# Performance work log

Hardware: AMD Instinct MI355X
Metric: run time of the kernel (lower is better)

## Reference

```python
import jax, jax.numpy as jnp
import numpy as np

USER_NUM, ITEM_NUM = 50000, 25000
N_U, N_I = 4096, 4096
N_E, N_PRED = 262144, 65536
D, K, N_LAYERS = 64, 1000, 3
SSL_TEMP, SSL_REG, ALPHA, PROTO_REG = 0.1, 1e-6, 1.0, 8e-8


def setup_inputs() -> dict:
    key = jax.random.key(0)
    ks = jax.random.split(key, 16)
    return {
        "emb_user": jax.random.normal(ks[0], (USER_NUM, D), jnp.float32),
        "emb_item": jax.random.normal(ks[1], (ITEM_NUM, D), jnp.float32),
        "user_centroids": jax.random.normal(ks[2], (K, D), jnp.float32),
        "item_centroids": jax.random.normal(ks[3], (K, D), jnp.float32),
        "edge_u": jax.random.randint(ks[4], (N_E,), 0, N_U, jnp.int32),
        "edge_v": jax.random.randint(ks[5], (N_E,), 0, N_I, jnp.int32),
        "pos_u": jax.random.randint(ks[6], (N_PRED,), 0, N_U, jnp.int32),
        "pos_v": jax.random.randint(ks[7], (N_PRED,), 0, N_I, jnp.int32),
        "neg_u": jax.random.randint(ks[8], (N_PRED,), 0, N_U, jnp.int32),
        "neg_v": jax.random.randint(ks[9], (N_PRED,), 0, N_I, jnp.int32),
        "idx_user": jax.random.randint(ks[10], (N_U,), 0, USER_NUM, jnp.int32),
        "idx_item": jax.random.randint(ks[11], (N_I,), 0, ITEM_NUM, jnp.int32),
        "user2cluster": jax.random.randint(ks[12], (USER_NUM,), 0, K, jnp.int32),
        "item2cluster": jax.random.randint(ks[13], (ITEM_NUM,), 0, K, jnp.int32),
    }


def _l2norm(x, eps=1e-12):  # F.normalize(p=2, dim=1)
    return x / jnp.maximum(jnp.linalg.norm(x, axis=1, keepdims=True), eps)


def _ssl_loss(cur, prev, prev_total):
    nc, npv, nt = _l2norm(cur), _l2norm(prev), _l2norm(prev_total)
    pos = jnp.exp(jnp.sum(nc * npv, axis=1) / SSL_TEMP)            # [B]
    tot = jnp.exp(nc @ nt.T / SSL_TEMP).sum(axis=1)                 # [B]
    return -jnp.log(pos / tot).sum()


def _proto_loss(emb, idx, node2cluster, centroids):
    ne = _l2norm(emb)
    cents = _l2norm(centroids)                                      # run_kmeans normalizes centroids
    my_cent = cents[node2cluster[idx]]                              # [B, D]
    pos = jnp.exp(jnp.sum(ne * my_cent, axis=1) / SSL_TEMP)
    tot = jnp.exp(ne @ cents.T / SSL_TEMP).sum(axis=1)
    return -jnp.log(pos / tot).sum()


def reference(emb_user, emb_item, user_centroids, item_centroids,
              edge_u, edge_v, pos_u, pos_v, neg_u, neg_v,
              idx_user, idx_item, user2cluster, item2cluster):
    # --- symmetric-normalized bipartite GraphConv (norm='both', no weight/bias) ---
    ones_e = jnp.ones((N_E,), jnp.float32)
    deg_u = jax.ops.segment_sum(ones_e, edge_u, num_segments=N_U)
    deg_i = jax.ops.segment_sum(ones_e, edge_v, num_segments=N_I)
    inv_u = (1.0 / jnp.sqrt(jnp.maximum(deg_u, 1.0)))[:, None]      # [N_U,1]
    inv_i = (1.0 / jnp.sqrt(jnp.maximum(deg_i, 1.0)))[:, None]      # [N_I,1]

    e_u = emb_user[idx_user]                                        # initial subgraph embeddings
    e_i = emb_item[idx_item]
    res_u, res_i = e_u, e_i
    h_u, h_i = e_u, e_i
    for _ in range(N_LAYERS):
        m_u = (h_u * inv_u)[edge_u]                                 # messages along rate edges
        m_i = (h_i * inv_i)[edge_v]                                 # messages along rated-by edges
        new_i = jax.ops.segment_sum(m_u, edge_v, num_segments=N_I) * inv_i
        new_u = jax.ops.segment_sum(m_i, edge_u, num_segments=N_U) * inv_u
        h_u, h_i = new_u, new_i
        res_u = res_u + h_u
        res_i = res_i + h_i

    # --- structural-neighbour SSL loss (last layer output vs layer-0 embeddings) ---
    ssl_u = _ssl_loss(h_u, e_u, emb_user)
    ssl_i = _ssl_loss(h_i, e_i, emb_item)
    ssl_loss = SSL_REG * (ssl_u + ALPHA * ssl_i)

    # --- protoNCE loss (raw embedding-table rows vs kmeans centroids) ---
    proto_loss = PROTO_REG * (
        _proto_loss(emb_user[idx_user], idx_user, user2cluster, user_centroids)
        + _proto_loss(emb_item[idx_item], idx_item, item2cluster, item_centroids)
    )

    res_u = res_u / (N_LAYERS + 1)
    res_i = res_i / (N_LAYERS + 1)

    # --- HeteroDotProductPredictor: u_dot_v on 'rate' edges -> [E,1] ---
    pos_score = jnp.sum(res_u[pos_u] * res_i[pos_v], axis=1, keepdims=True)
    neg_score = jnp.sum(res_u[neg_u] * res_i[neg_v], axis=1, keepdims=True)
    return pos_score, neg_score, ssl_loss, proto_loss
```

## Files before the change

### kernel.cpp

```cpp
#include <hip/hip_runtime.h>
#include <hip/hip_bf16.h>

#define NU 4096
#define NI 4096
#define NE 262144
#define NPRED 65536
#define DD 64
#define KCL 1000
#define UNUM 50000
#define INUM 25000
#define INUM_PAD 25008
#define KCL_PAD 1008

typedef short sh8 __attribute__((ext_vector_type(8)));
typedef float f4 __attribute__((ext_vector_type(4)));

__device__ __forceinline__ float wred64(float x){
#pragma unroll
  for(int m=1;m<64;m<<=1) x += __shfl_xor(x,m);
  return x;
}

__device__ __forceinline__ float fast_exp2(float x){
  return __builtin_amdgcn_exp2f(x);
}

__global__ void k_hist(const int* __restrict__ eu, const int* __restrict__ ev,
                       int* cu, int* ci){
  int t = blockIdx.x*256 + threadIdx.x;
  if(t < NE){ atomicAdd(&cu[eu[t]],1); atomicAdd(&ci[ev[t]],1); }
}

__global__ void k_scan(const int* cnt_u, int* rp_u, int* cur_u, float* inv_u,
                       const int* cnt_i, int* rp_i, int* cur_i, float* inv_i){
  const int* cnt = blockIdx.x ? cnt_i : cnt_u;
  int* rp  = blockIdx.x ? rp_i  : rp_u;
  int* cur = blockIdx.x ? cur_i : cur_u;
  float* inv = blockIdx.x ? inv_i : inv_u;
  __shared__ int sdata[1024];
  int tid = threadIdx.x;
  int v[4]; int s = 0;
#pragma unroll
  for(int k=0;k<4;k++){ v[k]=cnt[tid*4+k]; s+=v[k]; }
  sdata[tid]=s; __syncthreads();
  for(int off=1; off<1024; off<<=1){
    int add = (tid>=off)? sdata[tid-off] : 0;
    __syncthreads();
    if(tid>=off) sdata[tid] += add;
    __syncthreads();
  }
  int run = sdata[tid]-s;
#pragma unroll
  for(int k=0;k<4;k++){
    int idx = tid*4+k;
    rp[idx]=run; cur[idx]=run;
    inv[idx] = 1.0f/sqrtf(fmaxf((float)v[k],1.0f));
    run += v[k];
  }
  if(tid==1023) rp[4096]=run;
}

__global__ void k_fill(const int* __restrict__ eu, const int* __restrict__ ev,
                       int* cur_u, int* cur_i, int* adj_u, int* adj_i){
  int t = blockIdx.x*256 + threadIdx.x;
  if(t < NE){
    int u=eu[t], v=ev[t];
    adj_u[atomicAdd(&cur_u[u],1)] = v;
    adj_i[atomicAdd(&cur_i[v],1)] = u;
  }
}

__global__ void k_gather(const float* __restrict__ emb_u, const float* __restrict__ emb_i,
                         const int* __restrict__ idx_u, const int* __restrict__ idx_i,
                         const float* __restrict__ inv_u, const float* __restrict__ inv_i,
                         float* e_u, float* e_i, float* res_u, float* res_i,
                         float* hs_u, float* hs_i){
  int t = blockIdx.x*256 + threadIdx.x;
  const int half = NU*DD;
  if(t < half){
    int r=t>>6;
    float v = emb_u[idx_u[r]*DD + (t&63)];
    e_u[t]=v; res_u[t]=v; hs_u[t]=v*inv_u[r];
  } else {
    int s=t-half; int r=s>>6;
    float v = emb_i[idx_i[r]*DD + (s&63)];
    e_i[s]=v; res_i[s]=v; hs_i[s]=v*inv_i[r];
  }
}

__global__ void k_conv(const int* __restrict__ rp_i, const int* __restrict__ adj_i,
                       const float* __restrict__ hsu_in, const float* __restrict__ inv_i,
                       float* h_i, float* res_i, float* hsi_out,
                       const int* __restrict__ rp_u, const int* __restrict__ adj_u,
                       const float* __restrict__ hsi_in, const float* __restrict__ inv_u,
                       float* h_u, float* res_u, float* hsu_out){
  int b = blockIdx.x*4 + (threadIdx.x>>6);
  int lane = threadIdx.x & 63;
  const int* rp; const int* adj; const float* srcv; const float* inv;
  float *h, *res, *hso; int node;
  if(b < NI){ rp=rp_i; adj=adj_i; srcv=hsu_in; inv=inv_i; h=h_i; res=res_i; hso=hsi_out; node=b; }
  else      { node=b-NI; rp=rp_u; adj=adj_u; srcv=hsi_in; inv=inv_u; h=h_u; res=res_u; hso=hsu_out; }
  int s=rp[node], e=rp[node+1];
  float acc=0.f;
  for(int base=s; base<e; base+=64){
    int m = e-base;
    int myidx = adj[base + min(lane, m-1)];
    int kk = min(64, m);
    int k=0;
    for(; k+8<=kk; k+=8){
      int i0=__shfl(myidx,k  ), i1=__shfl(myidx,k+1),
          i2=__shfl(myidx,k+2), i3=__shfl(myidx,k+3),
          i4=__shfl(myidx,k+4), i5=__shfl(myidx,k+5),
          i6=__shfl(myidx,k+6), i7=__shfl(myidx,k+7);
      float v0=srcv[i0*DD+lane], v1=srcv[i1*DD+lane],
            v2=srcv[i2*DD+lane], v3=srcv[i3*DD+lane],
            v4=srcv[i4*DD+lane], v5=srcv[i5*DD+lane],
            v6=srcv[i6*DD+lane], v7=srcv[i7*DD+lane];
      acc += ((v0+v1)+(v2+v3)) + ((v4+v5)+(v6+v7));
    }
    for(; k<kk; k++) acc += srcv[__shfl(myidx,k)*DD+lane];
  }
  float iv = inv[node];
  float outv = acc*iv;
  h[node*DD+lane] = outv;
  res[node*DD+lane] += outv;
  hso[node*DD+lane] = outv*iv;
}

#define SB0 12500
#define SB1 (SB0+6252)
#define SB2 (SB1+252)
#define SB3 (SB2+252)
#define SB4 (SB3+1024)
#define SB5 (SB4+1024)
#define SB6 (SB5+1024)
#define SB7 (SB6+1024)

__global__ void k_normall(const float* __restrict__ emb_u, const float* __restrict__ emb_i,
                          const float* __restrict__ ucent, const float* __restrict__ icent,
                          const float* __restrict__ h_u, const float* __restrict__ h_i,
                          const float* __restrict__ e_u, const float* __restrict__ e_i,
                          __hip_bfloat16* ntb_u, __hip_bfloat16* ntb_i,
                          __hip_bfloat16* ncb_u, __hip_bfloat16* ncb_i,
                          __hip_bfloat16* nc_u, __hip_bfloat16* nc_i,
                          __hip_bfloat16* npv_u, __hip_bfloat16* npv_i){
  const float SC = 14.426950408889634f;
  int b = blockIdx.x;
  const float* in; __hip_bfloat16* outp; int rows; float scale; int base;
  if(b < SB0)      { in=emb_u; outp=ntb_u; rows=UNUM; scale=1.f;  base=0; }
  else if(b < SB1) { in=emb_i; outp=ntb_i; rows=INUM; scale=1.f;  base=SB0; }
  else if(b < SB2) { in=ucent; outp=ncb_u; rows=KCL;  scale=1.f;  base=SB1; }
  else if(b < SB3) { in=icent; outp=ncb_i; rows=KCL;  scale=1.f;  base=SB2; }
  else if(b < SB4) { in=h_u;   outp=nc_u;  rows=NU;   scale=SC;   base=SB3; }
  else if(b < SB5) { in=h_i;   outp=nc_i;  rows=NI;   scale=SC;   base=SB4; }
  else if(b < SB6) { in=e_u;   outp=npv_u; rows=NU;   scale=SC;   base=SB5; }
  else             { in=e_i;   outp=npv_i; rows=NI;   scale=SC;   base=SB6; }
  int row = (b-base)*4 + (threadIdx.x>>6);
  int lane = threadIdx.x & 63;
  if(row >= rows){
    outp[row*DD + lane] = __float2bfloat16(0.f);
    return;
  }
  float v = in[row*DD + lane];
  float s = wred64(v*v);
  float sc = scale / fmaxf(sqrtf(s), 1e-12f);
  outp[row*DD + lane] = __float2bfloat16(v*sc);
}

__global__ void k_pos(const float* __restrict__ h_u, const float* __restrict__ h_i,
                      const float* __restrict__ e_u, const float* __restrict__ e_i,
                      const float* __restrict__ cent_u, const float* __restrict__ cent_i,
                      const int* __restrict__ idx_u, const int* __restrict__ idx_i,
                      const int* __restrict__ u2c, const int* __restrict__ i2c,
                      float* pos4){
  int w = blockIdx.x*4 + (threadIdx.x>>6);
  int lane = threadIdx.x & 63;
  if(w >= NU) return;
  float hu=h_u[w*DD+lane], eu=e_u[w*DD+lane];
  float hi=h_i[w*DD+lane], ei=e_i[w*DD+lane];
  int cu = u2c[idx_u[w]], ci = i2c[idx_i[w]];
  float cuv = cent_u[cu*DD+lane], civ = cent_i[ci*DD+lane];
  float hh = wred64(hu*hu), ee = wred64(eu*eu), he = wred64(hu*eu);
  float h2 = wred64(hi*hi), e2 = wred64(ei*ei), hei= wred64(hi*ei);
  float ccu= wred64(cuv*cuv), ecu = wred64(eu*cuv);
  float cci= wred64(civ*civ), eci = wred64(ei*civ);
  if(lane==0){
    const float eps=1e-12f;
    pos4[0*NU+w] = he  / (fmaxf(sqrtf(hh),eps)*fmaxf(sqrtf(ee),eps));
    pos4[1*NU+w] = hei / (fmaxf(sqrtf(h2),eps)*fmaxf(sqrtf(e2),eps));
    pos4[2*NU+w] = ecu / (fmaxf(sqrtf(ee),eps)*fmaxf(sqrtf(ccu),eps));
    pos4[3*NU+w] = eci / (fmaxf(sqrtf(e2),eps)*fmaxf(sqrtf(cci),eps));
  }
}

#define ECH 256
#define EU0 1568
#define EU1 (EU0+784)
#define EU2 (EU1+32)
#define EU3 (EU2+32)

struct ESeg { const __hip_bfloat16* A; const __hip_bfloat16* B; float* tot; int nB; };

__global__ __launch_bounds__(256,4)
void k_expsum(ESeg s0, ESeg s1, ESeg s2, ESeg s3){
  int wave = threadIdx.x >> 6;
  int lane = threadIdx.x & 63;
  int r = lane & 15, kq = (lane>>4)*8;

  for(int u = blockIdx.x; u < EU3; u += 1024){
    ESeg s; int rem;
    if(u < EU0)      { s = s0; rem = u; }
    else if(u < EU1) { s = s1; rem = u-EU0; }
    else if(u < EU2) { s = s2; rem = u-EU1; }
    else             { s = s3; rem = u-EU2; }
    int yc = rem >> 3, x = rem & 7;
    int row0 = (x*4 + wave)*128;
    int j_begin = yc*ECH;
    int j_end = min(j_begin + ECH, s.nB);

    sh8 a0[8], a1[8];
#pragma unroll
    for(int t=0;t<8;t++){
      const short* ap = (const short*)(s.A + (row0 + t*16 + r)*DD);
      a0[t] = *(const sh8*)(ap + kq);
      a1[t] = *(const sh8*)(ap + kq + 32);
    }
    float acc[8][4];
#pragma unroll
    for(int t=0;t<8;t++)
#pragma unroll
      for(int q=0;q<4;q++) acc[t][q]=0.f;

    const short* bbase = (const short*)s.B;
    const short* bp0 = bbase + (j_begin + r)*DD + kq;
    sh8 b0 = *(const sh8*)(bp0);
    sh8 b1 = *(const sh8*)(bp0 + 32);

#pragma unroll 2
    for(int j0=j_begin; j0<j_end; j0+=16){
      const short* np = bbase + (j0 + 16 + r)*DD + kq;
      sh8 n0 = *(const sh8*)(np);
      sh8 n1 = *(const sh8*)(np + 32);
#pragma unroll
      for(int t=0;t<8;t++){
        f4 c = {0.f,0.f,0.f,0.f};
        c = __builtin_amdgcn_mfma_f32_16x16x32_bf16(a0[t], b0, c, 0,0,0);
        c = __builtin_amdgcn_mfma_f32_16x16x32_bf16(a1[t], b1, c, 0,0,0);
#pragma unroll
        for(int q=0;q<4;q++) acc[t][q] += fast_exp2(c[q]);
      }
      b0 = n0; b1 = n1;
    }
#pragma unroll
    for(int t=0;t<8;t++){
#pragma unroll
      for(int q=0;q<4;q++){
        float v = acc[t][q];
        v += __shfl_xor(v,1); v += __shfl_xor(v,2);
        v += __shfl_xor(v,4); v += __shfl_xor(v,8);
        if(r==0) atomicAdd(&s.tot[row0 + t*16 + (lane>>4)*4 + q], v);
      }
    }
  }
}

__global__ void k_score(const float* __restrict__ res_u, const float* __restrict__ res_i,
                        const int* __restrict__ pu, const int* __restrict__ pv,
                        const int* __restrict__ nu, const int* __restrict__ nv,
                        float* out){
  int t = blockIdx.x*256 + threadIdx.x;
  int pair = t >> 4;
  int sl = t & 15;
  if(pair >= 2*NPRED) return;
  int a,b;
  if(pair < NPRED){ a=pu[pair]; b=pv[pair]; }
  else { a=nu[pair-NPRED]; b=nv[pair-NPRED]; }
  f4 xu = *(const f4*)(res_u + a*DD + sl*4);
  f4 xv = *(const f4*)(res_i + b*DD + sl*4);
  float x = xu[0]*xv[0] + xu[1]*xv[1] + xu[2]*xv[2] + xu[3]*xv[3];
  x += __shfl_xor(x,1); x += __shfl_xor(x,2);
  x += __shfl_xor(x,4); x += __shfl_xor(x,8);
  if(sl==0) out[pair] = x*(1.0f/16.0f);
}

__global__ void k_loss(const float* __restrict__ tot4, const float* __restrict__ pos4,
                       float* out){
  const float PI_ = (float)(INUM_PAD-INUM), PK_ = (float)(KCL_PAD-KCL);
  float s0=0,s1=0,s2=0,s3=0;
  for(int b=threadIdx.x; b<NU; b+=256){
    s0 += logf(tot4[0*NU+b])       - 10.f*pos4[0*NU+b];
    s1 += logf(tot4[1*NU+b] - PI_) - 10.f*pos4[1*NU+b];
    s2 += logf(tot4[2*NU+b] - PK_) - 10.f*pos4[2*NU+b];
    s3 += logf(tot4[3*NU+b] - PK_) - 10.f*pos4[3*NU+b];
  }
  s0=wred64(s0); s1=wred64(s1); s2=wred64(s2); s3=wred64(s3);
  __shared__ float ls[4][4];
  int lane=threadIdx.x&63, w=threadIdx.x>>6;
  if(lane==0){ ls[w][0]=s0; ls[w][1]=s1; ls[w][2]=s2; ls[w][3]=s3; }
  __syncthreads();
  if(threadIdx.x==0){
    float a=0,b2=0,c=0,d=0;
#pragma unroll
    for(int k=0;k<4;k++){ a+=ls[k][0]; b2+=ls[k][1]; c+=ls[k][2]; d+=ls[k][3]; }
    out[2*NPRED]   = 1e-6f*(a+b2);
    out[2*NPRED+1] = 8e-8f*(c+d);
  }
}

extern "C" void kernel_launch(void* const* d_in, const int* in_sizes, int n_in,
                              void* d_out, int out_size, void* d_ws, size_t ws_size,
                              hipStream_t stream) {
  const float* emb_user = (const float*)d_in[0];
  const float* emb_item = (const float*)d_in[1];
  const float* ucent    = (const float*)d_in[2];
  const float* icent    = (const float*)d_in[3];
  const int* edge_u = (const int*)d_in[4];
  const int* edge_v = (const int*)d_in[5];
  const int* pos_u  = (const int*)d_in[6];
  const int* pos_v  = (const int*)d_in[7];
  const int* neg_u  = (const int*)d_in[8];
  const int* neg_v  = (const int*)d_in[9];
  const int* idx_u  = (const int*)d_in[10];
  const int* idx_i  = (const int*)d_in[11];
  const int* u2c    = (const int*)d_in[12];
  const int* i2c    = (const int*)d_in[13];
  float* out = (float*)d_out;

  char* w = (char*)d_ws;
  auto alloc = [&](size_t bytes)->void*{
    void* p = (void*)w;
    w += (bytes + 255) & ~(size_t)255;
    return p;
  };
  int* cnt_u = (int*)alloc(NU*4);
  int* cnt_i = (int*)alloc(NI*4);
  int* rp_u  = (int*)alloc((NU+1)*4);
  int* rp_i  = (int*)alloc((NI+1)*4);
  int* cur_u = (int*)alloc(NU*4);
  int* cur_i = (int*)alloc(NI*4);
  int* adj_u = (int*)alloc((size_t)NE*4);
  int* adj_i = (int*)alloc((size_t)NE*4);
  float* inv_u = (float*)alloc(NU*4);
  float* inv_i = (float*)alloc(NI*4);
  float* e_u  = (float*)alloc((size_t)NU*DD*4);
  float* e_i  = (float*)alloc((size_t)NI*DD*4);
  float* h_u  = (float*)alloc((size_t)NU*DD*4);
  float* h_i  = (float*)alloc((size_t)NI*DD*4);
  float* hsA_u = (float*)alloc((size_t)NU*DD*4);
  float* hsA_i = (float*)alloc((size_t)NI*DD*4);
  float* hsB_u = (float*)alloc((size_t)NU*DD*4);
  float* hsB_i = (float*)alloc((size_t)NI*DD*4);
  float* res_u= (float*)alloc((size_t)NU*DD*4);
  float* res_i= (float*)alloc((size_t)NI*DD*4);
  __hip_bfloat16* ntb_user = (__hip_bfloat16*)alloc((size_t)(UNUM+48)*DD*2);
  __hip_bfloat16* ntb_item = (__hip_bfloat16*)alloc((size_t)(INUM_PAD+48)*DD*2);
  __hip_bfloat16* ncb_u = (__hip_bfloat16*)alloc((size_t)(KCL_PAD+48)*DD*2);
  __hip_bfloat16* ncb_i = (__hip_bfloat16*)alloc((size_t)(KCL_PAD+48)*DD*2);
  __hip_bfloat16* nc_u  = (__hip_bfloat16*)alloc((size_t)NU*DD*2);
  __hip_bfloat16* nc_i  = (__hip_bfloat16*)alloc((size_t)NI*DD*2);
  __hip_bfloat16* npv_u = (__hip_bfloat16*)alloc((size_t)NU*DD*2);
  __hip_bfloat16* npv_i = (__hip_bfloat16*)alloc((size_t)NI*DD*2);
  float* tot4 = (float*)alloc(4*NU*4);
  float* pos4 = (float*)alloc(4*NU*4);

  hipMemsetAsync(cnt_u, 0, NU*4, stream);
  hipMemsetAsync(cnt_i, 0, NI*4, stream);
  hipMemsetAsync(tot4, 0, 4*NU*4, stream);

  k_hist<<<NE/256, 256, 0, stream>>>(edge_u, edge_v, cnt_u, cnt_i);
  k_scan<<<2, 1024, 0, stream>>>(cnt_u, rp_u, cur_u, inv_u, cnt_i, rp_i, cur_i, inv_i);
  k_fill<<<NE/256, 256, 0, stream>>>(edge_u, edge_v, cur_u, cur_i, adj_u, adj_i);
  k_gather<<<2*NU*DD/256, 256, 0, stream>>>(emb_user, emb_item, idx_u, idx_i,
                                            inv_u, inv_i,
                                            e_u, e_i, res_u, res_i, hsA_u, hsA_i);
  k_conv<<<(NU+NI)/4, 256, 0, stream>>>(rp_i, adj_i, hsA_u, inv_i, h_i, res_i, hsB_i,
                                        rp_u, adj_u, hsA_i, inv_u, h_u, res_u, hsB_u);
  k_conv<<<(NU+NI)/4, 256, 0, stream>>>(rp_i, adj_i, hsB_u, inv_i, h_i, res_i, hsA_i,
                                        rp_u, adj_u, hsB_i, inv_u, h_u, res_u, hsA_u);
  k_conv<<<(NU+NI)/4, 256, 0, stream>>>(rp_i, adj_i, hsA_u, inv_i, h_i, res_i, hsB_i,
                                        rp_u, adj_u, hsA_i, inv_u, h_u, res_u, hsB_u);

  k_normall<<<SB7, 256, 0, stream>>>(emb_user, emb_item, ucent, icent,
                                     h_u, h_i, e_u, e_i,
                                     ntb_user, ntb_item, ncb_u, ncb_i,
                                     nc_u, nc_i, npv_u, npv_i);

  k_pos<<<NU/4, 256, 0, stream>>>(h_u, h_i, e_u, e_i, ucent, icent,
                                  idx_u, idx_i, u2c, i2c, pos4);

  ESeg su = { nc_u,  ntb_user, tot4 + 0*NU, UNUM };
  ESeg si = { nc_i,  ntb_item, tot4 + 1*NU, INUM_PAD };
  ESeg sp0= { npv_u, ncb_u,    tot4 + 2*NU, KCL_PAD };
  ESeg sp1= { npv_i, ncb_i,    tot4 + 3*NU, KCL_PAD };
  k_expsum<<<1024, 256, 0, stream>>>(su, si, sp0, sp1);

  k_score<<<(2*NPRED*16)/256, 256, 0, stream>>>(res_u, res_i, pos_u, pos_v, neg_u, neg_v, out);
  k_loss<<<1, 256, 0, stream>>>(tot4, pos4, out);
}
```

Measured before the change: 241.2 us.

## Fuse small kernels and widen exp-sum inner loop to 32 columns

```diff
diff --git a/kernel.cpp b/kernel.cpp
--- a/kernel.cpp
+++ b/kernel.cpp
@@ -9,8 +9,9 @@
 #define KCL 1000
 #define UNUM 50000
 #define INUM 25000
-#define INUM_PAD 25008
-#define KCL_PAD 1008
+#define NUPAD 50016
+#define NIPAD 25024
+#define NKPAD 1024
 
 typedef short sh8 __attribute__((ext_vector_type(8)));
 typedef float f4 __attribute__((ext_vector_type(4)));
@@ -32,7 +33,13 @@
 }
 
 __global__ void k_scan(const int* cnt_u, int* rp_u, int* cur_u, float* inv_u,
-                       const int* cnt_i, int* rp_i, int* cur_i, float* inv_i){
+                       const int* cnt_i, int* rp_i, int* cur_i, float* inv_i,
+                       float* tot4){
+  {
+    int base = blockIdx.x*8192 + threadIdx.x*8;
+#pragma unroll
+    for(int k=0;k<8;k++) tot4[base+k] = 0.f;
+  }
   const int* cnt = blockIdx.x ? cnt_i : cnt_u;
   int* rp  = blockIdx.x ? rp_i  : rp_u;
   int* cur = blockIdx.x ? cur_i : cur_u;
@@ -60,31 +67,31 @@
   if(tid==1023) rp[4096]=run;
 }
 
-__global__ void k_fill(const int* __restrict__ eu, const int* __restrict__ ev,
-                       int* cur_u, int* cur_i, int* adj_u, int* adj_i){
-  int t = blockIdx.x*256 + threadIdx.x;
-  if(t < NE){
+__global__ void k_fillgather(const int* __restrict__ eu, const int* __restrict__ ev,
+                             int* cur_u, int* cur_i, int* adj_u, int* adj_i,
+                             const float* __restrict__ emb_u, const float* __restrict__ emb_i,
+                             const int* __restrict__ idx_u, const int* __restrict__ idx_i,
+                             const float* __restrict__ inv_u, const float* __restrict__ inv_i,
+                             float* e_u, float* e_i, float* res_u, float* res_i,
+                             float* hs_u, float* hs_i){
+  int b = blockIdx.x;
+  if(b < 1024){
+    int t = b*256 + threadIdx.x;
     int u=eu[t], v=ev[t];
     adj_u[atomicAdd(&cur_u[u],1)] = v;
     adj_i[atomicAdd(&cur_i[v],1)] = u;
-  }
-}
-
-__global__ void k_gather(const float* __restrict__ emb_u, const float* __restrict__ emb_i,
-                         const int* __restrict__ idx_u, const int* __restrict__ idx_i,
-                         const float* __restrict__ inv_u, const float* __restrict__ inv_i,
-                         float* e_u, float* e_i, float* res_u, float* res_i,
-                         float* hs_u, float* hs_i){
-  int t = blockIdx.x*256 + threadIdx.x;
-  const int half = NU*DD;
-  if(t < half){
-    int r=t>>6;
-    float v = emb_u[idx_u[r]*DD + (t&63)];
-    e_u[t]=v; res_u[t]=v; hs_u[t]=v*inv_u[r];
   } else {
-    int s=t-half; int r=s>>6;
-    float v = emb_i[idx_i[r]*DD + (s&63)];
-    e_i[s]=v; res_i[s]=v; hs_i[s]=v*inv_i[r];
+    int t = (b-1024)*256 + threadIdx.x;
+    const int half = NU*DD;
+    if(t < half){
+      int r=t>>6;
+      float v = emb_u[idx_u[r]*DD + (t&63)];
+      e_u[t]=v; res_u[t]=v; hs_u[t]=v*inv_u[r];
+    } else {
+      int s=t-half; int r=s>>6;
+      float v = emb_i[idx_i[r]*DD + (s&63)];
+      e_i[s]=v; res_i[s]=v; hs_i[s]=v*inv_i[r];
+    }
   }
 }
 
@@ -127,25 +134,48 @@
   hso[node*DD+lane] = outv*iv;
 }
 
-#define SB0 12500
-#define SB1 (SB0+6252)
-#define SB2 (SB1+252)
-#define SB3 (SB2+252)
+#define SB0 12504
+#define SB1 (SB0+6256)
+#define SB2 (SB1+256)
+#define SB3 (SB2+256)
 #define SB4 (SB3+1024)
 #define SB5 (SB4+1024)
 #define SB6 (SB5+1024)
 #define SB7 (SB6+1024)
 
-__global__ void k_normall(const float* __restrict__ emb_u, const float* __restrict__ emb_i,
+__global__ void k_normpos(const float* __restrict__ emb_u, const float* __restrict__ emb_i,
                           const float* __restrict__ ucent, const float* __restrict__ icent,
                           const float* __restrict__ h_u, const float* __restrict__ h_i,
                           const float* __restrict__ e_u, const float* __restrict__ e_i,
                           __hip_bfloat16* ntb_u, __hip_bfloat16* ntb_i,
                           __hip_bfloat16* ncb_u, __hip_bfloat16* ncb_i,
                           __hip_bfloat16* nc_u, __hip_bfloat16* nc_i,
-                          __hip_bfloat16* npv_u, __hip_bfloat16* npv_i){
+                          __hip_bfloat16* npv_u, __hip_bfloat16* npv_i,
+                          const int* __restrict__ idx_u, const int* __restrict__ idx_i,
+                          const int* __restrict__ u2c, const int* __restrict__ i2c,
+                          float* pos4){
   const float SC = 14.426950408889634f;
   int b = blockIdx.x;
+  int lane = threadIdx.x & 63;
+  if(b >= SB7){
+    int w = (b-SB7)*4 + (threadIdx.x>>6);
+    float hu=h_u[w*DD+lane], eu=e_u[w*DD+lane];
+    float hi=h_i[w*DD+lane], ei=e_i[w*DD+lane];
+    int cu = u2c[idx_u[w]], ci = i2c[idx_i[w]];
+    float cuv = ucent[cu*DD+lane], civ = icent[ci*DD+lane];
+    float hh = wred64(hu*hu), ee = wred64(eu*eu), he = wred64(hu*eu);
+    float h2 = wred64(hi*hi), e2 = wred64(ei*ei), hei= wred64(hi*ei);
+    float ccu= wred64(cuv*cuv), ecu = wred64(eu*cuv);
+    float cci= wred64(civ*civ), eci = wred64(ei*civ);
+    if(lane==0){
+      const float eps=1e-12f;
+      pos4[0*NU+w] = he  / (fmaxf(sqrtf(hh),eps)*fmaxf(sqrtf(ee),eps));
+      pos4[1*NU+w] = hei / (fmaxf(sqrtf(h2),eps)*fmaxf(sqrtf(e2),eps));
+      pos4[2*NU+w] = ecu / (fmaxf(sqrtf(ee),eps)*fmaxf(sqrtf(ccu),eps));
+      pos4[3*NU+w] = eci / (fmaxf(sqrtf(e2),eps)*fmaxf(sqrtf(cci),eps));
+    }
+    return;
+  }
   const float* in; __hip_bfloat16* outp; int rows; float scale; int base;
   if(b < SB0)      { in=emb_u; outp=ntb_u; rows=UNUM; scale=1.f;  base=0; }
   else if(b < SB1) { in=emb_i; outp=ntb_i; rows=INUM; scale=1.f;  base=SB0; }
@@ -156,7 +186,6 @@
   else if(b < SB6) { in=e_u;   outp=npv_u; rows=NU;   scale=SC;   base=SB5; }
   else             { in=e_i;   outp=npv_i; rows=NI;   scale=SC;   base=SB6; }
   int row = (b-base)*4 + (threadIdx.x>>6);
-  int lane = threadIdx.x & 63;
   if(row >= rows){
     outp[row*DD + lane] = __float2bfloat16(0.f);
     return;
@@ -167,128 +196,113 @@
   outp[row*DD + lane] = __float2bfloat16(v*sc);
 }
 
-__global__ void k_pos(const float* __restrict__ h_u, const float* __restrict__ h_i,
-                      const float* __restrict__ e_u, const float* __restrict__ e_i,
-                      const float* __restrict__ cent_u, const float* __restrict__ cent_i,
-                      const int* __restrict__ idx_u, const int* __restrict__ idx_i,
-                      const int* __restrict__ u2c, const int* __restrict__ i2c,
-                      float* pos4){
-  int w = blockIdx.x*4 + (threadIdx.x>>6);
-  int lane = threadIdx.x & 63;
-  if(w >= NU) return;
-  float hu=h_u[w*DD+lane], eu=e_u[w*DD+lane];
-  float hi=h_i[w*DD+lane], ei=e_i[w*DD+lane];
-  int cu = u2c[idx_u[w]], ci = i2c[idx_i[w]];
-  float cuv = cent_u[cu*DD+lane], civ = cent_i[ci*DD+lane];
-  float hh = wred64(hu*hu), ee = wred64(eu*eu), he = wred64(hu*eu);
-  float h2 = wred64(hi*hi), e2 = wred64(ei*ei), hei= wred64(hi*ei);
-  float ccu= wred64(cuv*cuv), ecu = wred64(eu*cuv);
-  float cci= wred64(civ*civ), eci = wred64(ei*civ);
-  if(lane==0){
-    const float eps=1e-12f;
-    pos4[0*NU+w] = he  / (fmaxf(sqrtf(hh),eps)*fmaxf(sqrtf(ee),eps));
-    pos4[1*NU+w] = hei / (fmaxf(sqrtf(h2),eps)*fmaxf(sqrtf(e2),eps));
-    pos4[2*NU+w] = ecu / (fmaxf(sqrtf(ee),eps)*fmaxf(sqrtf(ccu),eps));
-    pos4[3*NU+w] = eci / (fmaxf(sqrtf(e2),eps)*fmaxf(sqrtf(cci),eps));
-  }
-}
-
 #define ECH 256
-#define EU0 1568
-#define EU1 (EU0+784)
-#define EU2 (EU1+32)
-#define EU3 (EU2+32)
+#define EUU 1568
+#define EUI (EUU+784)
+#define EUP0 (EUI+32)
+#define EUP1 (EUP0+32)
+#define NSU 8192
+#define UTOT (EUP1+NSU)
 
 struct ESeg { const __hip_bfloat16* A; const __hip_bfloat16* B; float* tot; int nB; };
-
-__global__ __launch_bounds__(256,4)
-void k_expsum(ESeg s0, ESeg s1, ESeg s2, ESeg s3){
-  int wave = threadIdx.x >> 6;
-  int lane = threadIdx.x & 63;
+struct SArg { const float* res_u; const float* res_i;
+              const int* pu; const int* pv; const int* nu; const int* nv; float* out; };
+
+__global__ __launch_bounds__(256,3)
+void k_expscore(ESeg s0, ESeg s1, ESeg s2, ESeg s3, SArg sc){
+  int tid = threadIdx.x;
+  int wave = tid >> 6;
+  int lane = tid & 63;
   int r = lane & 15, kq = (lane>>4)*8;
 
-  for(int u = blockIdx.x; u < EU3; u += 1024){
-    ESeg s; int rem;
-    if(u < EU0)      { s = s0; rem = u; }
-    else if(u < EU1) { s = s1; rem = u-EU0; }
-    else if(u < EU2) { s = s2; rem = u-EU1; }
-    else             { s = s3; rem = u-EU2; }
-    int yc = rem >> 3, x = rem & 7;
-    int row0 = (x*4 + wave)*128;
-    int j_begin = yc*ECH;
-    int j_end = min(j_begin + ECH, s.nB);
-
-    sh8 a0[8], a1[8];
-#pragma unroll
-    for(int t=0;t<8;t++){
-      const short* ap = (const short*)(s.A + (row0 + t*16 + r)*DD);
-      a0[t] = *(const sh8*)(ap + kq);
-      a1[t] = *(const sh8*)(ap + kq + 32);
+  for(int u = blockIdx.x; u < UTOT; u += 1024){
+    if(u < EUP1){
+      ESeg s; int rem;
+      if(u < EUU)       { s = s0; rem = u; }
+      else if(u < EUI)  { s = s1; rem = u-EUU; }
+      else if(u < EUP0) { s = s2; rem = u-EUI; }
+      else              { s = s3; rem = u-EUP0; }
+      int yc = rem >> 3, x = rem & 7;
+      int row0 = (x*4 + wave)*128;
+      int j_begin = yc*ECH;
+      int j_end = min(j_begin + ECH, s.nB);
+
+      sh8 a0[8], a1[8];
+#pragma unroll
+      for(int t=0;t<8;t++){
+        const short* ap = (const short*)(s.A + (row0 + t*16 + r)*DD);
+        a0[t] = *(const sh8*)(ap + kq);
+        a1[t] = *(const sh8*)(ap + kq + 32);
+      }
+      float acc[8][4];
+#pragma unroll
+      for(int t=0;t<8;t++)
+#pragma unroll
+        for(int q=0;q<4;q++) acc[t][q]=0.f;
+
+      const short* bbase = (const short*)s.B;
+      const short* bp = bbase + (j_begin + r)*DD + kq;
+      sh8 b0 = *(const sh8*)(bp);
+      sh8 b1 = *(const sh8*)(bp + 32);
+      sh8 b2 = *(const sh8*)(bp + 16*DD);
+      sh8 b3 = *(const sh8*)(bp + 16*DD + 32);
+
+#pragma unroll 1
+      for(int j0=j_begin; j0<j_end; j0+=32){
+        const short* np = bbase + (j0 + 32 + r)*DD + kq;
+        sh8 n0 = *(const sh8*)(np);
+        sh8 n1 = *(const sh8*)(np + 32);
+        sh8 n2 = *(const sh8*)(np + 16*DD);
+        sh8 n3 = *(const sh8*)(np + 16*DD + 32);
+#pragma unroll
+        for(int t=0;t<8;t++){
+          f4 c0 = {0.f,0.f,0.f,0.f};
+          f4 c1 = {0.f,0.f,0.f,0.f};
+          c0 = __builtin_amdgcn_mfma_f32_16x16x32_bf16(a0[t], b0, c0, 0,0,0);
+          c1 = __builtin_amdgcn_mfma_f32_16x16x32_bf16(a0[t], b2, c1, 0,0,0);
+          c0 = __builtin_amdgcn_mfma_f32_16x16x32_bf16(a1[t], b1, c0, 0,0,0);
+          c1 = __builtin_amdgcn_mfma_f32_16x16x32_bf16(a1[t], b3, c1, 0,0,0);
+#pragma unroll
+          for(int q=0;q<4;q++)
+            acc[t][q] += fast_exp2(c0[q]) + fast_exp2(c1[q]);
+        }
+        b0 = n0; b1 = n1; b2 = n2; b3 = n3;
+      }
+#pragma unroll
+      for(int t=0;t<8;t++){
+#pragma unroll
+        for(int q=0;q<4;q++){
+          float v = acc[t][q];
+          v += __shfl_xor(v,1); v += __shfl_xor(v,2);
+          v += __shfl_xor(v,4); v += __shfl_xor(v,8);
+          if(r==0) atomicAdd(&s.tot[row0 + t*16 + (lane>>4)*4 + q], v);
+        }
+      }
+    } else {
+      int u2 = u - EUP1;
+      int pair = u2*16 + (tid>>4);
+      int sl = tid & 15;
+      int a,b;
+      if(pair < NPRED){ a=sc.pu[pair]; b=sc.pv[pair]; }
+      else { a=sc.nu[pair-NPRED]; b=sc.nv[pair-NPRED]; }
+      f4 xu = *(const f4*)(sc.res_u + a*DD + sl*4);
+      f4 xv = *(const f4*)(sc.res_i + b*DD + sl*4);
+      float x = xu[0]*xv[0] + xu[1]*xv[1] + xu[2]*xv[2] + xu[3]*xv[3];
+      x += __shfl_xor(x,1); x += __shfl_xor(x,2);
+      x += __shfl_xor(x,4); x += __shfl_xor(x,8);
+      if(sl==0) sc.out[pair] = x*(1.0f/16.0f);
     }
-    float acc[8][4];
-#pragma unroll
-    for(int t=0;t<8;t++)
-#pragma unroll
-      for(int q=0;q<4;q++) acc[t][q]=0.f;
-
-    const short* bbase = (const short*)s.B;
-    const short* bp0 = bbase + (j_begin + r)*DD + kq;
-    sh8 b0 = *(const sh8*)(bp0);
-    sh8 b1 = *(const sh8*)(bp0 + 32);
-
-#pragma unroll 2
-    for(int j0=j_begin; j0<j_end; j0+=16){
-      const short* np = bbase + (j0 + 16 + r)*DD + kq;
-      sh8 n0 = *(const sh8*)(np);
-      sh8 n1 = *(const sh8*)(np + 32);
-#pragma unroll
-      for(int t=0;t<8;t++){
-        f4 c = {0.f,0.f,0.f,0.f};
-        c = __builtin_amdgcn_mfma_f32_16x16x32_bf16(a0[t], b0, c, 0,0,0);
-        c = __builtin_amdgcn_mfma_f32_16x16x32_bf16(a1[t], b1, c, 0,0,0);
-#pragma unroll
-        for(int q=0;q<4;q++) acc[t][q] += fast_exp2(c[q]);
-      }
-      b0 = n0; b1 = n1;
-    }
-#pragma unroll
-    for(int t=0;t<8;t++){
-#pragma unroll
-      for(int q=0;q<4;q++){
-        float v = acc[t][q];
-        v += __shfl_xor(v,1); v += __shfl_xor(v,2);
-        v += __shfl_xor(v,4); v += __shfl_xor(v,8);
-        if(r==0) atomicAdd(&s.tot[row0 + t*16 + (lane>>4)*4 + q], v);
-      }
-    }
-  }
-}
-
-__global__ void k_score(const float* __restrict__ res_u, const float* __restrict__ res_i,
-                        const int* __restrict__ pu, const int* __restrict__ pv,
-                        const int* __restrict__ nu, const int* __restrict__ nv,
-                        float* out){
-  int t = blockIdx.x*256 + threadIdx.x;
-  int pair = t >> 4;
-  int sl = t & 15;
-  if(pair >= 2*NPRED) return;
-  int a,b;
-  if(pair < NPRED){ a=pu[pair]; b=pv[pair]; }
-  else { a=nu[pair-NPRED]; b=nv[pair-NPRED]; }
-  f4 xu = *(const f4*)(res_u + a*DD + sl*4);
-  f4 xv = *(const f4*)(res_i + b*DD + sl*4);
-  float x = xu[0]*xv[0] + xu[1]*xv[1] + xu[2]*xv[2] + xu[3]*xv[3];
-  x += __shfl_xor(x,1); x += __shfl_xor(x,2);
-  x += __shfl_xor(x,4); x += __shfl_xor(x,8);
-  if(sl==0) out[pair] = x*(1.0f/16.0f);
+  }
 }
 
 __global__ void k_loss(const float* __restrict__ tot4, const float* __restrict__ pos4,
                        float* out){
-  const float PI_ = (float)(INUM_PAD-INUM), PK_ = (float)(KCL_PAD-KCL);
+  const float PU_ = (float)(NUPAD-UNUM);
+  const float PI_ = (float)(NIPAD-INUM);
+  const float PK_ = (float)(NKPAD-KCL);
   float s0=0,s1=0,s2=0,s3=0;
   for(int b=threadIdx.x; b<NU; b+=256){
-    s0 += logf(tot4[0*NU+b])       - 10.f*pos4[0*NU+b];
+    s0 += logf(tot4[0*NU+b] - PU_) - 10.f*pos4[0*NU+b];
     s1 += logf(tot4[1*NU+b] - PI_) - 10.f*pos4[1*NU+b];
     s2 += logf(tot4[2*NU+b] - PK_) - 10.f*pos4[2*NU+b];
     s3 += logf(tot4[3*NU+b] - PK_) - 10.f*pos4[3*NU+b];
@@ -352,10 +366,10 @@
   float* hsB_i = (float*)alloc((size_t)NI*DD*4);
   float* res_u= (float*)alloc((size_t)NU*DD*4);
   float* res_i= (float*)alloc((size_t)NI*DD*4);
-  __hip_bfloat16* ntb_user = (__hip_bfloat16*)alloc((size_t)(UNUM+48)*DD*2);
-  __hip_bfloat16* ntb_item = (__hip_bfloat16*)alloc((size_t)(INUM_PAD+48)*DD*2);
-  __hip_bfloat16* ncb_u = (__hip_bfloat16*)alloc((size_t)(KCL_PAD+48)*DD*2);
-  __hip_bfloat16* ncb_i = (__hip_bfloat16*)alloc((size_t)(KCL_PAD+48)*DD*2);
+  __hip_bfloat16* ntb_user = (__hip_bfloat16*)alloc((size_t)(NUPAD+64)*DD*2);
+  __hip_bfloat16* ntb_item = (__hip_bfloat16*)alloc((size_t)(NIPAD+64)*DD*2);
+  __hip_bfloat16* ncb_u = (__hip_bfloat16*)alloc((size_t)(NKPAD+64)*DD*2);
+  __hip_bfloat16* ncb_i = (__hip_bfloat16*)alloc((size_t)(NKPAD+64)*DD*2);
   __hip_bfloat16* nc_u  = (__hip_bfloat16*)alloc((size_t)NU*DD*2);
   __hip_bfloat16* nc_i  = (__hip_bfloat16*)alloc((size_t)NI*DD*2);
   __hip_bfloat16* npv_u = (__hip_bfloat16*)alloc((size_t)NU*DD*2);
@@ -363,16 +377,15 @@
   float* tot4 = (float*)alloc(4*NU*4);
   float* pos4 = (float*)alloc(4*NU*4);
 
-  hipMemsetAsync(cnt_u, 0, NU*4, stream);
-  hipMemsetAsync(cnt_i, 0, NI*4, stream);
-  hipMemsetAsync(tot4, 0, 4*NU*4, stream);
+  hipMemsetAsync(cnt_u, 0, 2*NU*4, stream);
 
   k_hist<<<NE/256, 256, 0, stream>>>(edge_u, edge_v, cnt_u, cnt_i);
-  k_scan<<<2, 1024, 0, stream>>>(cnt_u, rp_u, cur_u, inv_u, cnt_i, rp_i, cur_i, inv_i);
-  k_fill<<<NE/256, 256, 0, stream>>>(edge_u, edge_v, cur_u, cur_i, adj_u, adj_i);
-  k_gather<<<2*NU*DD/256, 256, 0, stream>>>(emb_user, emb_item, idx_u, idx_i,
-                                            inv_u, inv_i,
-                                            e_u, e_i, res_u, res_i, hsA_u, hsA_i);
+  k_scan<<<2, 1024, 0, stream>>>(cnt_u, rp_u, cur_u, inv_u,
+                                 cnt_i, rp_i, cur_i, inv_i, tot4);
+  k_fillgather<<<3072, 256, 0, stream>>>(edge_u, edge_v, cur_u, cur_i, adj_u, adj_i,
+                                         emb_user, emb_item, idx_u, idx_i,
+                                         inv_u, inv_i,
+                                         e_u, e_i, res_u, res_i, hsA_u, hsA_i);
   k_conv<<<(NU+NI)/4, 256, 0, stream>>>(rp_i, adj_i, hsA_u, inv_i, h_i, res_i, hsB_i,
                                         rp_u, adj_u, hsA_i, inv_u, h_u, res_u, hsB_u);
   k_conv<<<(NU+NI)/4, 256, 0, stream>>>(rp_i, adj_i, hsB_u, inv_i, h_i, res_i, hsA_i,
@@ -380,20 +393,18 @@
   k_conv<<<(NU+NI)/4, 256, 0, stream>>>(rp_i, adj_i, hsA_u, inv_i, h_i, res_i, hsB_i,
                                         rp_u, adj_u, hsA_i, inv_u, h_u, res_u, hsB_u);
 
-  k_normall<<<SB7, 256, 0, stream>>>(emb_user, emb_item, ucent, icent,
-                                     h_u, h_i, e_u, e_i,
-                                     ntb_user, ntb_item, ncb_u, ncb_i,
-                                     nc_u, nc_i, npv_u, npv_i);
-
-  k_pos<<<NU/4, 256, 0, stream>>>(h_u, h_i, e_u, e_i, ucent, icent,
-                                  idx_u, idx_i, u2c, i2c, pos4);
-
-  ESeg su = { nc_u,  ntb_user, tot4 + 0*NU, UNUM };
-  ESeg si = { nc_i,  ntb_item, tot4 + 1*NU, INUM_PAD };
-  ESeg sp0= { npv_u, ncb_u,    tot4 + 2*NU, KCL_PAD };
-  ESeg sp1= { npv_i, ncb_i,    tot4 + 3*NU, KCL_PAD };
-  k_expsum<<<1024, 256, 0, stream>>>(su, si, sp0, sp1);
-
-  k_score<<<(2*NPRED*16)/256, 256, 0, stream>>>(res_u, res_i, pos_u, pos_v, neg_u, neg_v, out);
+  k_normpos<<<SB7+NU/4, 256, 0, stream>>>(emb_user, emb_item, ucent, icent,
+                                          h_u, h_i, e_u, e_i,
+                                          ntb_user, ntb_item, ncb_u, ncb_i,
+                                          nc_u, nc_i, npv_u, npv_i,
+                                          idx_u, idx_i, u2c, i2c, pos4);
+
+  ESeg su = { nc_u,  ntb_user, tot4 + 0*NU, NUPAD };
+  ESeg si = { nc_i,  ntb_item, tot4 + 1*NU, NIPAD };
+  ESeg sp0= { npv_u, ncb_u,    tot4 + 2*NU, NKPAD };
+  ESeg sp1= { npv_i, ncb_i,    tot4 + 3*NU, NKPAD };
+  SArg sc = { res_u, res_i, pos_u, pos_v, neg_u, neg_v, out };
+  k_expscore<<<1024, 256, 0, stream>>>(su, si, sp0, sp1, sc);
+
   k_loss<<<1, 256, 0, stream>>>(tot4, pos4, out);
 }
```

New measurement: 257.5 us. 1.07x slower.
